# Performance work log

Measured on AMD Instinct MI355X. Metric: run time of the kernel, lower is better.

The kernel has to match this reference:

```python
import jax, jax.numpy as jnp
import numpy as np

H = 16
D_MODEL = 1024
D_K = D_MODEL // H
NWORDS = 16384


def setup_inputs() -> dict:
    key0 = jax.random.key(0)
    ks = jax.random.split(key0, 11)
    s = 0.02
    return {
        "query": jax.random.normal(ks[0], (1, D_MODEL), dtype=jnp.float32),
        "key": jax.random.normal(ks[1], (NWORDS, D_MODEL), dtype=jnp.float32),
        "value": jax.random.normal(ks[2], (NWORDS, D_MODEL), dtype=jnp.float32),
        "Wq": jax.random.normal(ks[3], (D_MODEL, D_MODEL), dtype=jnp.float32) * s,
        "bq": jax.random.normal(ks[4], (D_MODEL,), dtype=jnp.float32) * s,
        "Wk": jax.random.normal(ks[5], (D_MODEL, D_MODEL), dtype=jnp.float32) * s,
        "bk": jax.random.normal(ks[6], (D_MODEL,), dtype=jnp.float32) * s,
        "Wv": jax.random.normal(ks[7], (D_MODEL, D_MODEL), dtype=jnp.float32) * s,
        "bv": jax.random.normal(ks[8], (D_MODEL,), dtype=jnp.float32) * s,
        "Wo": jax.random.normal(ks[9], (D_MODEL, D_MODEL), dtype=jnp.float32) * s,
        "bo": jax.random.normal(ks[10], (D_MODEL,), dtype=jnp.float32) * s,
    }


def reference(query, key, value, Wq, bq, Wk, bk, Wv, bv, Wo, bo):
    # torch Linear: y = x @ W.T + b
    q = (query @ Wq.T + bq).reshape(H, D_K)          # [h, d_k]  (single query token)
    k = (key @ Wk.T + bk).reshape(-1, H, D_K)        # [n, h, d_k]
    v = (value @ Wv.T + bv).reshape(-1, H, D_K)      # [n, h, d_k]
    # NOTE: original module applies NO 1/sqrt(d_k) scaling.
    scores = jnp.einsum("hd,nhd->hn", q, k)          # [h, n]
    p_attn = jax.nn.softmax(scores, axis=-1)          # dropout p=0 -> no-op
    x = jnp.einsum("hn,nhd->hd", p_attn, v).reshape(1, H * D_K)  # [1, d_model]
    return x @ Wo.T + bo                              # [1, d_model]
```

## Files before the change

### kernel.cpp

```cpp
#include <hip/hip_runtime.h>

#define DM 1024
#define NW 16384

typedef __attribute__((ext_vector_type(8))) short short8;
typedef __attribute__((ext_vector_type(4))) float f32x4;

#define OFF_AH   1024
#define OFF_AL   9216
#define OFF_D0   17408
#define OFF_S    17424
#define OFF_X    17696
#define OFF_W    18720
#define OFF_E    36864
#define OFF_PART 299008

__device__ __forceinline__ unsigned short f2bf(float f) {
  unsigned int u = __float_as_uint(f);
  return (unsigned short)((u + 0x7fffu + ((u >> 16) & 1u)) >> 16);
}

__global__ __launch_bounds__(256) void k_rowdot(const float* __restrict__ W,
                                                const float* __restrict__ v,
                                                const float* __restrict__ b,
                                                float* __restrict__ out) {
  const int wave = (blockIdx.x * 256 + threadIdx.x) >> 6;
  const int lane = threadIdx.x & 63;
  const float* row = W + (size_t)wave * DM + 4 * lane;
  float s = 0.f;
#pragma unroll
  for (int j = 0; j < 4; ++j) {
    float4 a = *(const float4*)(row + j * 256);
    float4 x = *(const float4*)(v + j * 256 + 4 * lane);
    s += a.x * x.x + a.y * x.y + a.z * x.z + a.w * x.w;
  }
#pragma unroll
  for (int off = 32; off; off >>= 1) s += __shfl_xor(s, off, 64);
  if (lane == 0) out[wave] = s + b[wave];
}

__global__ __launch_bounds__(256) void k_qck(const float* __restrict__ Wq,
                                             const float* __restrict__ bq,
                                             const float* __restrict__ query,
                                             const float* __restrict__ Wk,
                                             const float* __restrict__ bk,
                                             short* __restrict__ Ah,
                                             short* __restrict__ Al,
                                             float* __restrict__ d0,
                                             float* __restrict__ S) {
  const int h = blockIdx.x >> 2;
  const int mc = blockIdx.x & 3;
  const int t = threadIdx.x;
  const int lane = t & 63;
  const int wv = t >> 6;
  __shared__ float qh[64];
  if (blockIdx.x == 0 && t < 16) S[t] = 0.f;
  float4 qv[4];
#pragma unroll
  for (int j = 0; j < 4; ++j) qv[j] = *(const float4*)(query + j * 256 + 4 * lane);
#pragma unroll 1
  for (int i = 0; i < 16; i += 2) {
    const int d0i = 4 * i + wv;
    const int d1i = 4 * (i + 1) + wv;
    const float* r0 = Wq + (size_t)(h * 64 + d0i) * DM + 4 * lane;
    const float* r1 = Wq + (size_t)(h * 64 + d1i) * DM + 4 * lane;
    float4 a0[4], a1[4];
#pragma unroll
    for (int j = 0; j < 4; ++j) { a0[j] = *(const float4*)(r0 + j * 256);
                                  a1[j] = *(const float4*)(r1 + j * 256); }
    float s0 = 0.f, s1 = 0.f;
#pragma unroll
    for (int j = 0; j < 4; ++j) {
      s0 += a0[j].x * qv[j].x + a0[j].y * qv[j].y + a0[j].z * qv[j].z + a0[j].w * qv[j].w;
      s1 += a1[j].x * qv[j].x + a1[j].y * qv[j].y + a1[j].z * qv[j].z + a1[j].w * qv[j].w;
    }
#pragma unroll
    for (int off = 32; off; off >>= 1) { s0 += __shfl_xor(s0, off, 64);
                                         s1 += __shfl_xor(s1, off, 64); }
    if (lane == 0) { qh[d0i] = s0 + bq[h * 64 + d0i];
                     qh[d1i] = s1 + bq[h * 64 + d1i]; }
  }
  __syncthreads();
  const int m = mc * 256 + t;
  const float* Wp = Wk + (size_t)(h * 64) * DM + m;
  float s = 0.f;
#pragma unroll 1
  for (int db = 0; db < 8; ++db) {
    float wv8[8];
#pragma unroll
    for (int j = 0; j < 8; ++j) wv8[j] = Wp[(size_t)(db * 8 + j) * DM];
#pragma unroll
    for (int j = 0; j < 8; ++j) s = fmaf(qh[db * 8 + j], wv8[j], s);
  }
  unsigned short hu = f2bf(s);
  float hf = __uint_as_float(((unsigned int)hu) << 16);
  unsigned short lu = f2bf(s - hf);
  const int kb = m >> 5, q = (m >> 3) & 3, j = m & 7;
  const int idx = (kb * 64 + q * 16 + h) * 8 + j;
  Ah[idx] = (short)hu;
  Al[idx] = (short)lu;
  if (mc == 0 && t == 0) {
    float tt = 0.f;
    for (int d = 0; d < 64; ++d) tt += qh[d] * bk[h * 64 + d];
    d0[h] = tt;
  }
}

__global__ __launch_bounds__(64, 1) void k_scores(const float* __restrict__ key,
                                                  const short* __restrict__ AhG,
                                                  const short* __restrict__ AlG,
                                                  const float* __restrict__ d0,
                                                  float* __restrict__ e) {
  const int tile = blockIdx.x;
  const int lane = threadIdx.x;
  const int n = tile * 16 + (lane & 15);
  const int quad = lane >> 4;
  const float* base = key + (size_t)n * DM + quad * 8;
  const short8* A8h = (const short8*)AhG;
  const short8* A8l = (const short8*)AlG;

  short8 ah[2][4], al[2][4];
  float4 f0[2][4], f1[2][4];
  f32x4 acc0 = {0.f, 0.f, 0.f, 0.f};
  f32x4 acc1 = {0.f, 0.f, 0.f, 0.f};

#define LOADG(buf, g) { \
  _Pragma("unroll") for (int i = 0; i < 4; ++i) { \
    const int kb = (g) * 4 + i; \
    ah[buf][i] = A8h[kb * 64 + lane]; \
    al[buf][i] = A8l[kb * 64 + lane]; \
    f0[buf][i] = *(const float4*)(base + kb * 32); \
    f1[buf][i] = *(const float4*)(base + kb * 32 + 4); \
  } }

#define PROC(buf) { \
  _Pragma("unroll") for (int i = 0; i < 4; ++i) { \
    float ff[8] = {f0[buf][i].x, f0[buf][i].y, f0[buf][i].z, f0[buf][i].w, \
                   f1[buf][i].x, f1[buf][i].y, f1[buf][i].z, f1[buf][i].w}; \
    short8 bh, bl; \
    _Pragma("unroll") for (int j = 0; j < 8; ++j) { \
      unsigned short hu = f2bf(ff[j]); \
      bh[j] = (short)hu; \
      float hf = __uint_as_float(((unsigned int)hu) << 16); \
      bl[j] = (short)f2bf(ff[j] - hf); \
    } \
    if ((i & 1) == 0) { \
      acc0 = __builtin_amdgcn_mfma_f32_16x16x32_bf16(ah[buf][i], bh, acc0, 0, 0, 0); \
      acc0 = __builtin_amdgcn_mfma_f32_16x16x32_bf16(ah[buf][i], bl, acc0, 0, 0, 0); \
      acc0 = __builtin_amdgcn_mfma_f32_16x16x32_bf16(al[buf][i], bh, acc0, 0, 0, 0); \
    } else { \
      acc1 = __builtin_amdgcn_mfma_f32_16x16x32_bf16(ah[buf][i], bh, acc1, 0, 0, 0); \
      acc1 = __builtin_amdgcn_mfma_f32_16x16x32_bf16(ah[buf][i], bl, acc1, 0, 0, 0); \
      acc1 = __builtin_amdgcn_mfma_f32_16x16x32_bf16(al[buf][i], bh, acc1, 0, 0, 0); \
    } \
  } }

  LOADG(0, 0)
  LOADG(1, 1)
  PROC(0) LOADG(0, 2)
  PROC(1) LOADG(1, 3)
  PROC(0) LOADG(0, 4)
  PROC(1) LOADG(1, 5)
  PROC(0) LOADG(0, 6)
  PROC(1) LOADG(1, 7)
  PROC(0)
  PROC(1)
#undef LOADG
#undef PROC

  const float4 dv = *(const float4*)(d0 + quad * 4);
  float ex0 = __expf(acc0[0] + acc1[0] + dv.x);
  float ex1 = __expf(acc0[1] + acc1[1] + dv.y);
  float ex2 = __expf(acc0[2] + acc1[2] + dv.z);
  float ex3 = __expf(acc0[3] + acc1[3] + dv.w);
  *(float4*)(e + (size_t)n * 16 + quad * 4) = make_float4(ex0, ex1, ex2, ex3);
}

__global__ __launch_bounds__(256, 2) void k_pv(const float* __restrict__ value,
                                               const float* __restrict__ e,
                                               float* __restrict__ part,
                                               float* __restrict__ S) {
  const int nb = blockIdx.x >> 2;
  const int mc = blockIdx.x & 3;
  const int t = threadIdx.x;
  const int lane = t & 63;
  const int wy = t >> 6;
  const int col = mc * 256 + lane * 4;
  const int n0 = nb * 128;
  __shared__ float el[128 * 16];
  __shared__ float4 red[2][16][64];
  __shared__ float sp[4][16];
  {
    const float4* eg = (const float4*)(e + (size_t)n0 * 16);
    float4* es = (float4*)el;
#pragma unroll
    for (int k = 0; k < 2; ++k) es[t + k * 256] = eg[t + k * 256];
  }
  __syncthreads();
  if (mc == 0) {
    const int h = t & 15;
    const int rg = t >> 4;
    float p = 0.f;
#pragma unroll
    for (int j = 0; j < 8; ++j) p += el[(rg * 8 + j) * 16 + h];
    p += __shfl_xor(p, 16, 64);
    p += __shfl_xor(p, 32, 64);
    if (lane < 16) sp[wy][lane] = p;
    __syncthreads();
    if (t < 16) atomicAdd(S + t, sp[0][t] + sp[1][t] + sp[2][t] + sp[3][t]);
  }
  float4 acc[16];
#pragma unroll
  for (int h = 0; h < 16; ++h) acc[h] = make_float4(0.f, 0.f, 0.f, 0.f);
  const float* vp = value + (size_t)(n0 + wy * 32) * DM + col;
  const float* ep = &el[wy * 32 * 16];
#pragma unroll 1
  for (int rb = 0; rb < 4; ++rb) {
    float4 v[8];
#pragma unroll
    for (int i = 0; i < 8; ++i) v[i] = *(const float4*)(vp + (size_t)(rb * 8 + i) * DM);
#pragma unroll
    for (int i = 0; i < 8; ++i) {
      const float4* er4 = (const float4*)(ep + (rb * 8 + i) * 16);
      float4 e0 = er4[0], e1 = er4[1], e2 = er4[2], e3 = er4[3];
      float4 vv = v[i];
#define FMA4H(H, P) { acc[H].x = fmaf(P, vv.x, acc[H].x); acc[H].y = fmaf(P, vv.y, acc[H].y); \
                      acc[H].z = fmaf(P, vv.z, acc[H].z); acc[H].w = fmaf(P, vv.w, acc[H].w); }
      FMA4H(0,  e0.x) FMA4H(1,  e0.y) FMA4H(2,  e0.z) FMA4H(3,  e0.w)
      FMA4H(4,  e1.x) FMA4H(5,  e1.y) FMA4H(6,  e1.z) FMA4H(7,  e1.w)
      FMA4H(8,  e2.x) FMA4H(9,  e2.y) FMA4H(10, e2.z) FMA4H(11, e2.w)
      FMA4H(12, e3.x) FMA4H(13, e3.y) FMA4H(14, e3.z) FMA4H(15, e3.w)
#undef FMA4H
    }
  }
  if (wy >= 2) {
#pragma unroll
    for (int h = 0; h < 16; ++h) red[wy - 2][h][lane] = acc[h];
  }
  __syncthreads();
  if (wy < 2) {
#pragma unroll
    for (int h = 0; h < 16; ++h) {
      float4 o = red[wy][h][lane];
      acc[h].x += o.x; acc[h].y += o.y; acc[h].z += o.z; acc[h].w += o.w;
    }
  }
  __syncthreads();
  if (wy == 1) {
#pragma unroll
    for (int h = 0; h < 16; ++h) red[0][h][lane] = acc[h];
  }
  __syncthreads();
  if (wy == 0) {
    float* pp = part + (size_t)nb * (16 * DM) + col;
#pragma unroll
    for (int h = 0; h < 16; ++h) {
      float4 o = red[0][h][lane];
      acc[h].x += o.x; acc[h].y += o.y; acc[h].z += o.z; acc[h].w += o.w;
      *(float4*)(pp + (size_t)h * DM) = acc[h];
    }
  }
}

__global__ __launch_bounds__(256) void k_wred(const float* __restrict__ part,
                                              float* __restrict__ w) {
  const int gid = blockIdx.x * 256 + threadIdx.x;
  const int o = gid >> 2;
  const int q = gid & 3;
  float s = 0.f;
#pragma unroll
  for (int ib = 0; ib < 4; ++ib) {
    float x[8];
#pragma unroll
    for (int j = 0; j < 8; ++j) x[j] = part[(size_t)(q * 32 + ib * 8 + j) * 16384 + o];
#pragma unroll
    for (int j = 0; j < 8; ++j) s += x[j];
  }
  s += __shfl_xor(s, 1, 64);
  s += __shfl_xor(s, 2, 64);
  if (q == 0) w[o] = s;
}

__global__ __launch_bounds__(256) void k_xproj(const float* __restrict__ Wv,
                                               const float* __restrict__ w,
                                               const float* __restrict__ bv,
                                               const float* __restrict__ S,
                                               float* __restrict__ x) {
  const int wave = (blockIdx.x * 256 + threadIdx.x) >> 6;
  const int lane = threadIdx.x & 63;
  const int h = wave >> 6;
  const float* vec = w + (size_t)h * DM;
  const float* row = Wv + (size_t)wave * DM + 4 * lane;
  float s = 0.f;
#pragma unroll
  for (int j = 0; j < 4; ++j) {
    float4 a = *(const float4*)(row + j * 256);
    float4 x4 = *(const float4*)(vec + j * 256 + 4 * lane);
    s += a.x * x4.x + a.y * x4.y + a.z * x4.z + a.w * x4.w;
  }
#pragma unroll
  for (int off = 32; off; off >>= 1) s += __shfl_xor(s, off, 64);
  if (lane == 0) x[wave] = s / S[h] + bv[wave];
}

extern "C" void kernel_launch(void* const* d_in, const int* in_sizes, int n_in,
                              void* d_out, int out_size, void* d_ws, size_t ws_size,
                              hipStream_t stream) {
  const float* query = (const float*)d_in[0];
  const float* key   = (const float*)d_in[1];
  const float* value = (const float*)d_in[2];
  const float* Wq    = (const float*)d_in[3];
  const float* bq    = (const float*)d_in[4];
  const float* Wk    = (const float*)d_in[5];
  const float* bk    = (const float*)d_in[6];
  const float* Wv    = (const float*)d_in[7];
  const float* bv    = (const float*)d_in[8];
  const float* Wo    = (const float*)d_in[9];
  const float* bo    = (const float*)d_in[10];
  float* out = (float*)d_out;
  float* ws  = (float*)d_ws;
  short* Ah  = (short*)(ws + OFF_AH);
  short* Al  = (short*)(ws + OFF_AL);

  k_qck    <<<64,  256, 0, stream>>>(Wq, bq, query, Wk, bk, Ah, Al, ws + OFF_D0, ws + OFF_S);
  k_scores <<<1024, 64, 0, stream>>>(key, Ah, Al, ws + OFF_D0, ws + OFF_E);
  k_pv     <<<512, 256, 0, stream>>>(value, ws + OFF_E, ws + OFF_PART, ws + OFF_S);
  k_wred   <<<256, 256, 0, stream>>>(ws + OFF_PART, ws + OFF_W);
  k_xproj  <<<256, 256, 0, stream>>>(Wv, ws + OFF_W, bv, ws + OFF_S, ws + OFF_X);
  k_rowdot <<<256, 256, 0, stream>>>(Wo, ws + OFF_X, bo, out);
}
```

Before: 216.2 us.

## Fuse score and PV kernels, keep exp scores in shared memory

Merges the MFMA score kernel and the P·V accumulation kernel into one kernel. Each 256-thread block scores 64 keys, stores the exponentials in LDS, then accumulates all 1024 value columns for those rows, which removes the global round trip of e and one launch. The Wq projection loop now handles four rows per iteration, and the partial reduction splits across blocks using atomics into w, which is zeroed in k_qck. In exchange, grid parallelism drops to 256 blocks of one wave-set each, and atomic float sums become nondeterministic.

```diff
diff --git a/kernel.cpp b/kernel.cpp
--- a/kernel.cpp
+++ b/kernel.cpp
@@ -12,8 +12,7 @@
 #define OFF_S    17424
 #define OFF_X    17696
 #define OFF_W    18720
-#define OFF_E    36864
-#define OFF_PART 299008
+#define OFF_PART 36864
 
 __device__ __forceinline__ unsigned short f2bf(float f) {
   unsigned int u = __float_as_uint(f);
@@ -47,7 +46,8 @@
                                              short* __restrict__ Ah,
                                              short* __restrict__ Al,
                                              float* __restrict__ d0,
-                                             float* __restrict__ S) {
+                                             float* __restrict__ S,
+                                             float* __restrict__ w) {
   const int h = blockIdx.x >> 2;
   const int mc = blockIdx.x & 3;
   const int t = threadIdx.x;
@@ -55,36 +55,40 @@
   const int wv = t >> 6;
   __shared__ float qh[64];
   if (blockIdx.x == 0 && t < 16) S[t] = 0.f;
+  w[blockIdx.x * 256 + t] = 0.f;
   float4 qv[4];
 #pragma unroll
   for (int j = 0; j < 4; ++j) qv[j] = *(const float4*)(query + j * 256 + 4 * lane);
 #pragma unroll 1
-  for (int i = 0; i < 16; i += 2) {
-    const int d0i = 4 * i + wv;
-    const int d1i = 4 * (i + 1) + wv;
-    const float* r0 = Wq + (size_t)(h * 64 + d0i) * DM + 4 * lane;
-    const float* r1 = Wq + (size_t)(h * 64 + d1i) * DM + 4 * lane;
-    float4 a0[4], a1[4];
-#pragma unroll
-    for (int j = 0; j < 4; ++j) { a0[j] = *(const float4*)(r0 + j * 256);
-                                  a1[j] = *(const float4*)(r1 + j * 256); }
-    float s0 = 0.f, s1 = 0.f;
-#pragma unroll
-    for (int j = 0; j < 4; ++j) {
-      s0 += a0[j].x * qv[j].x + a0[j].y * qv[j].y + a0[j].z * qv[j].z + a0[j].w * qv[j].w;
-      s1 += a1[j].x * qv[j].x + a1[j].y * qv[j].y + a1[j].z * qv[j].z + a1[j].w * qv[j].w;
+  for (int ii = 0; ii < 16; ii += 4) {
+    float4 a[4][4];
+#pragma unroll
+    for (int r = 0; r < 4; ++r) {
+      const float* rp = Wq + (size_t)(h * 64 + 4 * (ii + r) + wv) * DM + 4 * lane;
+#pragma unroll
+      for (int j = 0; j < 4; ++j) a[r][j] = *(const float4*)(rp + j * 256);
     }
-#pragma unroll
-    for (int off = 32; off; off >>= 1) { s0 += __shfl_xor(s0, off, 64);
-                                         s1 += __shfl_xor(s1, off, 64); }
-    if (lane == 0) { qh[d0i] = s0 + bq[h * 64 + d0i];
-                     qh[d1i] = s1 + bq[h * 64 + d1i]; }
+    float s[4] = {0.f, 0.f, 0.f, 0.f};
+#pragma unroll
+    for (int r = 0; r < 4; ++r)
+#pragma unroll
+      for (int j = 0; j < 4; ++j)
+        s[r] += a[r][j].x * qv[j].x + a[r][j].y * qv[j].y +
+                a[r][j].z * qv[j].z + a[r][j].w * qv[j].w;
+#pragma unroll
+    for (int off = 32; off; off >>= 1)
+#pragma unroll
+      for (int r = 0; r < 4; ++r) s[r] += __shfl_xor(s[r], off, 64);
+    if (lane == 0)
+#pragma unroll
+      for (int r = 0; r < 4; ++r)
+        qh[4 * (ii + r) + wv] = s[r] + bq[h * 64 + 4 * (ii + r) + wv];
   }
   __syncthreads();
   const int m = mc * 256 + t;
   const float* Wp = Wk + (size_t)(h * 64) * DM + m;
   float s = 0.f;
-#pragma unroll 1
+#pragma unroll 2
   for (int db = 0; db < 8; ++db) {
     float wv8[8];
 #pragma unroll
@@ -106,18 +110,24 @@
   }
 }
 
-__global__ __launch_bounds__(64, 1) void k_scores(const float* __restrict__ key,
-                                                  const short* __restrict__ AhG,
-                                                  const short* __restrict__ AlG,
-                                                  const float* __restrict__ d0,
-                                                  float* __restrict__ e) {
-  const int tile = blockIdx.x;
-  const int lane = threadIdx.x;
-  const int n = tile * 16 + (lane & 15);
+__global__ __launch_bounds__(256, 1) void k_spv(const float* __restrict__ key,
+                                                const float* __restrict__ value,
+                                                const short* __restrict__ AhG,
+                                                const short* __restrict__ AlG,
+                                                const float* __restrict__ d0,
+                                                float* __restrict__ part,
+                                                float* __restrict__ S) {
+  const int nb = blockIdx.x;
+  const int t = threadIdx.x;
+  const int lane = t & 63;
+  const int wv = t >> 6;
+  const int nl = wv * 16 + (lane & 15);
+  const int n = nb * 64 + nl;
   const int quad = lane >> 4;
   const float* base = key + (size_t)n * DM + quad * 8;
   const short8* A8h = (const short8*)AhG;
   const short8* A8l = (const short8*)AlG;
+  __shared__ float el[64 * 16];
 
   short8 ah[2][4], al[2][4];
   float4 f0[2][4], f1[2][4];
@@ -168,60 +178,28 @@
 #undef LOADG
 #undef PROC
 
-  const float4 dv = *(const float4*)(d0 + quad * 4);
-  float ex0 = __expf(acc0[0] + acc1[0] + dv.x);
-  float ex1 = __expf(acc0[1] + acc1[1] + dv.y);
-  float ex2 = __expf(acc0[2] + acc1[2] + dv.z);
-  float ex3 = __expf(acc0[3] + acc1[3] + dv.w);
-  *(float4*)(e + (size_t)n * 16 + quad * 4) = make_float4(ex0, ex1, ex2, ex3);
-}
-
-__global__ __launch_bounds__(256, 2) void k_pv(const float* __restrict__ value,
-                                               const float* __restrict__ e,
-                                               float* __restrict__ part,
-                                               float* __restrict__ S) {
-  const int nb = blockIdx.x >> 2;
-  const int mc = blockIdx.x & 3;
-  const int t = threadIdx.x;
-  const int lane = t & 63;
-  const int wy = t >> 6;
-  const int col = mc * 256 + lane * 4;
-  const int n0 = nb * 128;
-  __shared__ float el[128 * 16];
-  __shared__ float4 red[2][16][64];
-  __shared__ float sp[4][16];
   {
-    const float4* eg = (const float4*)(e + (size_t)n0 * 16);
-    float4* es = (float4*)el;
-#pragma unroll
-    for (int k = 0; k < 2; ++k) es[t + k * 256] = eg[t + k * 256];
+    const float4 dv = *(const float4*)(d0 + quad * 4);
+    float ex0 = __expf(acc0[0] + acc1[0] + dv.x);
+    float ex1 = __expf(acc0[1] + acc1[1] + dv.y);
+    float ex2 = __expf(acc0[2] + acc1[2] + dv.z);
+    float ex3 = __expf(acc0[3] + acc1[3] + dv.w);
+    *(float4*)&el[nl * 16 + quad * 4] = make_float4(ex0, ex1, ex2, ex3);
   }
   __syncthreads();
-  if (mc == 0) {
-    const int h = t & 15;
-    const int rg = t >> 4;
-    float p = 0.f;
-#pragma unroll
-    for (int j = 0; j < 8; ++j) p += el[(rg * 8 + j) * 16 + h];
-    p += __shfl_xor(p, 16, 64);
-    p += __shfl_xor(p, 32, 64);
-    if (lane < 16) sp[wy][lane] = p;
-    __syncthreads();
-    if (t < 16) atomicAdd(S + t, sp[0][t] + sp[1][t] + sp[2][t] + sp[3][t]);
-  }
+
   float4 acc[16];
 #pragma unroll
   for (int h = 0; h < 16; ++h) acc[h] = make_float4(0.f, 0.f, 0.f, 0.f);
-  const float* vp = value + (size_t)(n0 + wy * 32) * DM + col;
-  const float* ep = &el[wy * 32 * 16];
+  const float* vp = value + (size_t)(nb * 64) * DM + 4 * t;
 #pragma unroll 1
-  for (int rb = 0; rb < 4; ++rb) {
+  for (int rb = 0; rb < 8; ++rb) {
     float4 v[8];
 #pragma unroll
     for (int i = 0; i < 8; ++i) v[i] = *(const float4*)(vp + (size_t)(rb * 8 + i) * DM);
 #pragma unroll
     for (int i = 0; i < 8; ++i) {
-      const float4* er4 = (const float4*)(ep + (rb * 8 + i) * 16);
+      const float4* er4 = (const float4*)&el[(rb * 8 + i) * 16];
       float4 e0 = er4[0], e1 = er4[1], e2 = er4[2], e3 = er4[3];
       float4 vv = v[i];
 #define FMA4H(H, P) { acc[H].x = fmaf(P, vv.x, acc[H].x); acc[H].y = fmaf(P, vv.y, acc[H].y); \
@@ -233,52 +211,34 @@
 #undef FMA4H
     }
   }
-  if (wy >= 2) {
-#pragma unroll
-    for (int h = 0; h < 16; ++h) red[wy - 2][h][lane] = acc[h];
-  }
-  __syncthreads();
-  if (wy < 2) {
-#pragma unroll
-    for (int h = 0; h < 16; ++h) {
-      float4 o = red[wy][h][lane];
-      acc[h].x += o.x; acc[h].y += o.y; acc[h].z += o.z; acc[h].w += o.w;
-    }
-  }
-  __syncthreads();
-  if (wy == 1) {
-#pragma unroll
-    for (int h = 0; h < 16; ++h) red[0][h][lane] = acc[h];
-  }
-  __syncthreads();
-  if (wy == 0) {
-    float* pp = part + (size_t)nb * (16 * DM) + col;
-#pragma unroll
-    for (int h = 0; h < 16; ++h) {
-      float4 o = red[0][h][lane];
-      acc[h].x += o.x; acc[h].y += o.y; acc[h].z += o.z; acc[h].w += o.w;
-      *(float4*)(pp + (size_t)h * DM) = acc[h];
-    }
+  float* pp = part + (size_t)nb * (16 * DM) + 4 * t;
+#pragma unroll
+  for (int h = 0; h < 16; ++h) *(float4*)(pp + (size_t)h * DM) = acc[h];
+
+  if (t < 16) {
+    float s = 0.f;
+#pragma unroll
+    for (int r = 0; r < 64; ++r) s += el[r * 16 + t];
+    atomicAdd(S + t, s);
   }
 }
 
 __global__ __launch_bounds__(256) void k_wred(const float* __restrict__ part,
                                               float* __restrict__ w) {
-  const int gid = blockIdx.x * 256 + threadIdx.x;
-  const int o = gid >> 2;
-  const int q = gid & 3;
-  float s = 0.f;
-#pragma unroll
-  for (int ib = 0; ib < 4; ++ib) {
+  const int g = blockIdx.x * 256 + threadIdx.x;
+  const int o = g & 16383;
+  const int q = g >> 14;
+  float s = 0.f;
+#pragma unroll 1
+  for (int ib = 0; ib < 8; ++ib) {
     float x[8];
 #pragma unroll
-    for (int j = 0; j < 8; ++j) x[j] = part[(size_t)(q * 32 + ib * 8 + j) * 16384 + o];
+    for (int j = 0; j < 8; ++j)
+      x[j] = part[(size_t)(q * 64 + ib * 8 + j) * 16384 + o];
 #pragma unroll
     for (int j = 0; j < 8; ++j) s += x[j];
   }
-  s += __shfl_xor(s, 1, 64);
-  s += __shfl_xor(s, 2, 64);
-  if (q == 0) w[o] = s;
+  atomicAdd(w + o, s);
 }
 
 __global__ __launch_bounds__(256) void k_xproj(const float* __restrict__ Wv,
@@ -322,9 +282,10 @@
   short* Ah  = (short*)(ws + OFF_AH);
   short* Al  = (short*)(ws + OFF_AL);
 
-  k_qck    <<<64,  256, 0, stream>>>(Wq, bq, query, Wk, bk, Ah, Al, ws + OFF_D0, ws + OFF_S);
-  k_scores <<<1024, 64, 0, stream>>>(key, Ah, Al, ws + OFF_D0, ws + OFF_E);
-  k_pv     <<<512, 256, 0, stream>>>(value, ws + OFF_E, ws + OFF_PART, ws + OFF_S);
+  k_qck    <<<64,  256, 0, stream>>>(Wq, bq, query, Wk, bk, Ah, Al,
+                                     ws + OFF_D0, ws + OFF_S, ws + OFF_W);
+  k_spv    <<<256, 256, 0, stream>>>(key, value, Ah, Al, ws + OFF_D0,
+                                     ws + OFF_PART, ws + OFF_S);
   k_wred   <<<256, 256, 0, stream>>>(ws + OFF_PART, ws + OFF_W);
   k_xproj  <<<256, 256, 0, stream>>>(Wv, ws + OFF_W, bv, ws + OFF_S, ws + OFF_X);
   k_rowdot <<<256, 256, 0, stream>>>(Wo, ws + OFF_X, bo, out);
```

Result: no change. 216.9 us (+0.3%).
